# Kernel optimization log

Hardware: AMD Instinct MI355X
Metric: run time of the kernel (lower is better)

## Reference

```python
import jax, jax.numpy as jnp
import numpy as np

N = 50000        # nodes
E = 800000       # edges (before self loops)
IN = 128         # in_channels
HID = 32         # hidden_channels (per head)
HEADS = 4
OUT = 10         # out_channels (classes)
G = 64           # graphs in batch
NEG_SLOPE = 0.2  # PyG GATConv default leaky relu slope


def setup_inputs() -> dict:
    key = jax.random.key(0)
    ks = jax.random.split(key, 12)
    s = 0.05
    return {
        "x": jax.random.normal(ks[0], (N, IN), jnp.float32),
        "W1": jax.random.normal(ks[1], (IN, HEADS * HID), jnp.float32) * s,
        "a1_src": jax.random.normal(ks[2], (HEADS, HID), jnp.float32) * s,
        "a1_dst": jax.random.normal(ks[3], (HEADS, HID), jnp.float32) * s,
        "b1": jnp.zeros((HEADS * HID,), jnp.float32),
        "W2": jax.random.normal(ks[4], (HEADS * HID, HEADS * HID), jnp.float32) * s,
        "a2_src": jax.random.normal(ks[5], (HEADS, HID), jnp.float32) * s,
        "a2_dst": jax.random.normal(ks[6], (HEADS, HID), jnp.float32) * s,
        "b2": jnp.zeros((HEADS * HID,), jnp.float32),
        "Wl": jax.random.normal(ks[7], (HEADS * HID, OUT), jnp.float32) * s,
        "bl": jnp.zeros((OUT,), jnp.float32),
        "edge_index": jax.random.randint(ks[8], (2, E), 0, N, jnp.int32),
        "batch": jnp.sort(jax.random.randint(ks[9], (N,), 0, G, jnp.int32)),
    }


def gat_conv(x, src, dst, W, a_src, a_dst, b):
    """PyG GATConv (concat=True, self loops already in src/dst). Eval mode: no dropout."""
    n = x.shape[0]
    h = (x @ W).reshape(n, HEADS, HID)                       # [N,H,C]
    al_s = jnp.einsum('nhc,hc->nh', h, a_src)                # [N,H]
    al_d = jnp.einsum('nhc,hc->nh', h, a_dst)
    e = jax.nn.leaky_relu(al_s[src] + al_d[dst], NEG_SLOPE)  # [Etot,H]
    # segment softmax over destination node neighborhoods
    m = jax.ops.segment_max(e, dst, num_segments=n)
    m = jnp.where(jnp.isfinite(m), m, 0.0)
    p = jnp.exp(e - m[dst])
    z = jax.ops.segment_sum(p, dst, num_segments=n)
    alpha = p / (z[dst] + 1e-16)                             # [Etot,H]
    out = jax.ops.segment_sum(h[src] * alpha[:, :, None], dst, num_segments=n)
    return out.reshape(n, HEADS * HID) + b


def reference(x, W1, a1_src, a1_dst, b1, W2, a2_src, a2_dst, b2, Wl, bl,
              edge_index, batch):
    n = x.shape[0]
    loops = jnp.arange(n, dtype=edge_index.dtype)
    src = jnp.concatenate([edge_index[0], loops])
    dst = jnp.concatenate([edge_index[1], loops])

    h = jax.nn.elu(gat_conv(x, src, dst, W1, a1_src, a1_dst, b1))
    h = gat_conv(h, src, dst, W2, a2_src, a2_dst, b2)

    # global_mean_pool over graph ids
    counts = jax.ops.segment_sum(jnp.ones((n,), h.dtype), batch, num_segments=G)
    pooled = jax.ops.segment_sum(h, batch, num_segments=G) / jnp.maximum(counts, 1.0)[:, None]

    logits = pooled @ Wl + bl
    return jax.nn.softmax(logits, axis=1)
```

## Files before the change

kernel.cpp:

```cpp
#include <hip/hip_runtime.h>
#include <hip/hip_bf16.h>
#include <math.h>

#define HEADS 4
#define HID 32
#define FDIM 128
#define OUTC 10
#define NEG 0.2f
#define ECAP 512

typedef __attribute__((ext_vector_type(4))) float f32x4;
typedef __attribute__((ext_vector_type(8))) short bf16x8;

static __device__ __forceinline__ float lrelu(float v) { return v > 0.f ? v : NEG * v; }

static __device__ __forceinline__ unsigned bfr(float f) {
  unsigned u = __float_as_uint(f);
  return (u + 0x7fffu + ((u >> 16) & 1u)) >> 16;
}
static __device__ __forceinline__ float blo(unsigned u) { return __uint_as_float(u << 16); }
static __device__ __forceinline__ float bhi(unsigned u) { return __uint_as_float(u & 0xffff0000u); }

#define CHUNK 4096

__global__ __launch_bounds__(256) void k_bhist(
    const int* __restrict__ ei, int* __restrict__ gbc, int E, int n, int nb) {
  __shared__ int h[256];
  h[threadIdx.x] = 0;
  __syncthreads();
  int base = blockIdx.x * CHUNK;
  int tot = E + n;
  #pragma unroll
  for (int r = 0; r < 16; ++r) {
    int e = base + r * 256 + threadIdx.x;
    if (e < tot) {
      int dst = (e < E) ? ei[E + e] : (e - E);
      atomicAdd(&h[dst >> 8], 1);
    }
  }
  __syncthreads();
  if (threadIdx.x < nb && h[threadIdx.x]) atomicAdd(&gbc[threadIdx.x], h[threadIdx.x]);
}

__global__ void k_bscan(const int* __restrict__ gbc, int* __restrict__ bbase,
                        int* __restrict__ gbcur, int nb) {
  __shared__ int sh[256];
  int v = (threadIdx.x < nb) ? gbc[threadIdx.x] : 0;
  sh[threadIdx.x] = v;
  __syncthreads();
  #pragma unroll
  for (int off = 1; off < 256; off <<= 1) {
    int t = (threadIdx.x >= off) ? sh[threadIdx.x - off] : 0;
    __syncthreads();
    sh[threadIdx.x] += t;
    __syncthreads();
  }
  int excl = sh[threadIdx.x] - v;
  if (threadIdx.x <= nb) bbase[threadIdx.x] = excl;
  if (threadIdx.x < nb) gbcur[threadIdx.x] = excl;
}

__global__ __launch_bounds__(256) void k_bin(
    const int* __restrict__ ei, int* __restrict__ gbcur,
    int2* __restrict__ bbuf, int E, int n) {
  __shared__ int h[256];
  __shared__ int cur[256];
  h[threadIdx.x] = 0;
  __syncthreads();
  int base = blockIdx.x * CHUNK;
  int tot = E + n;
  #pragma unroll
  for (int r = 0; r < 16; ++r) {
    int e = base + r * 256 + threadIdx.x;
    if (e < tot) {
      int dst = (e < E) ? ei[E + e] : (e - E);
      atomicAdd(&h[dst >> 8], 1);
    }
  }
  __syncthreads();
  if (h[threadIdx.x]) cur[threadIdx.x] = atomicAdd(&gbcur[threadIdx.x], h[threadIdx.x]);
  __syncthreads();
  #pragma unroll
  for (int r = 0; r < 16; ++r) {
    int e = base + r * 256 + threadIdx.x;
    if (e < tot) {
      int src = (e < E) ? ei[e] : (e - E);
      int dst = (e < E) ? ei[E + e] : (e - E);
      int pos = atomicAdd(&cur[dst >> 8], 1);
      bbuf[pos] = make_int2(src, dst);
    }
  }
}

__global__ __launch_bounds__(256) void k_build(
    const int2* __restrict__ bbuf, const int* __restrict__ bbase,
    int* __restrict__ offs, int* __restrict__ csr, int* __restrict__ dpos,
    int n, int nb) {
  __shared__ int deg[256];
  __shared__ int sc[256];
  __shared__ int cur[256];
  int b = blockIdx.x;
  int ebeg = bbase[b], eend = bbase[b + 1];
  deg[threadIdx.x] = 0;
  __syncthreads();
  for (int i = ebeg + threadIdx.x; i < eend; i += 256)
    atomicAdd(&deg[bbuf[i].y & 255], 1);
  __syncthreads();
  int v = deg[threadIdx.x];
  sc[threadIdx.x] = v;
  __syncthreads();
  #pragma unroll
  for (int off = 1; off < 256; off <<= 1) {
    int t = (threadIdx.x >= off) ? sc[threadIdx.x - off] : 0;
    __syncthreads();
    sc[threadIdx.x] += t;
    __syncthreads();
  }
  int excl = sc[threadIdx.x] - v;
  int dst0 = b * 256 + threadIdx.x;
  if (dst0 < n) offs[dst0] = ebeg + excl;
  if (b == 0 && threadIdx.x == 0) offs[n] = bbase[nb];
  cur[threadIdx.x] = ebeg + excl;
  __syncthreads();
  for (int i = ebeg + threadIdx.x; i < eend; i += 256) {
    int2 sd = bbuf[i];
    int pos = atomicAdd(&cur[sd.y & 255], 1);
    csr[pos] = sd.x;
    dpos[pos] = sd.y;
  }
}

__global__ void k_wa(const float* __restrict__ W1, const float* __restrict__ W2,
                     const float* __restrict__ a1s, const float* __restrict__ a1d,
                     const float* __restrict__ a2s, const float* __restrict__ a2d,
                     float* __restrict__ Wa) {
  int layer = blockIdx.y;
  const float* W = layer ? W2 : W1;
  int c = blockIdx.x;
  int k = threadIdx.x;
  int h = c & 3;
  const float* av = (c < 4 ? (layer ? a2s : a1s) : (layer ? a2d : a1d)) + h * 32;
  const float* wr = W + (size_t)k * 128 + h * 32;
  float s = 0.f;
  #pragma unroll
  for (int j = 0; j < 32; j += 4) {
    float4 wv = *reinterpret_cast<const float4*>(wr + j);
    float4 a4 = *reinterpret_cast<const float4*>(av + j);
    s += wv.x * a4.x + wv.y * a4.y + wv.z * a4.z + wv.w * a4.w;
  }
  Wa[layer * 1024 + k * 8 + c] = s;
}

__global__ void k_prep(const float* __restrict__ W1, const float* __restrict__ W2,
                       const float* __restrict__ Wa, uint4* __restrict__ WF) {
  int layer = blockIdx.y;
  const float* W = layer ? W2 : W1;
  const float* wa = Wa + layer * 1024;
  int gid = blockIdx.x * 256 + threadIdx.x;
  if (gid >= 2304) return;
  int lane = gid & 63, frag = gid >> 6;
  int t = frag / 9, ct = frag - t * 9;
  int quad = lane >> 4, r = lane & 15;
  int kbase = t * 32 + quad * 8;
  unsigned v[8];
  if (ct < 8) {
    int col = ct * 16 + r;
    #pragma unroll
    for (int j = 0; j < 8; ++j) v[j] = bfr(W[(size_t)(kbase + j) * 128 + col]);
  } else if (r < 8) {
    #pragma unroll
    for (int j = 0; j < 8; ++j) v[j] = bfr(wa[(kbase + j) * 8 + r]);
  } else {
    #pragma unroll
    for (int j = 0; j < 8; ++j) v[j] = 0;
  }
  uint4 pk;
  pk.x = v[0] | (v[1] << 16);
  pk.y = v[2] | (v[3] << 16);
  pk.z = v[4] | (v[5] << 16);
  pk.w = v[6] | (v[7] << 16);
  WF[layer * 2304 + gid] = pk;
}

template<bool BF16IN>
__global__ __launch_bounds__(256) void k_mm(
    const void* __restrict__ Xv, const uint4* __restrict__ WF,
    unsigned short* __restrict__ H, float* __restrict__ AL, int n) {
  __shared__ uint4 wf[2304];
  int tid = threadIdx.x;
  #pragma unroll
  for (int i = 0; i < 9; ++i) wf[i * 256 + tid] = WF[i * 256 + tid];
  __syncthreads();
  int lane = tid & 63, wid = tid >> 6;
  int quad = lane >> 4, r = lane & 15;
  int rowbase = blockIdx.x * 64 + wid * 16;
  int arow = rowbase + r;
  int arowc = arow < n ? arow : 0;
  const bf16x8* wfs = (const bf16x8*)wf;

  f32x4 acc[9];
  #pragma unroll
  for (int ct = 0; ct < 9; ++ct) acc[ct] = 0;

  #pragma unroll
  for (int t = 0; t < 4; ++t) {
    bf16x8 a;
    if (BF16IN) {
      const uint4* xp = reinterpret_cast<const uint4*>(Xv) + (size_t)arowc * 16;
      uint4 u = xp[t * 4 + quad];
      a = *reinterpret_cast<const bf16x8*>(&u);
    } else {
      const float* xp = reinterpret_cast<const float*>(Xv) + (size_t)arowc * 128 + quad * 8;
      float4 x0 = *reinterpret_cast<const float4*>(xp + t * 32);
      float4 x1 = *reinterpret_cast<const float4*>(xp + t * 32 + 4);
      a[0] = (short)bfr(x0.x); a[1] = (short)bfr(x0.y);
      a[2] = (short)bfr(x0.z); a[3] = (short)bfr(x0.w);
      a[4] = (short)bfr(x1.x); a[5] = (short)bfr(x1.y);
      a[6] = (short)bfr(x1.z); a[7] = (short)bfr(x1.w);
    }
    #pragma unroll
    for (int ct = 0; ct < 9; ++ct)
      acc[ct] = __builtin_amdgcn_mfma_f32_16x16x32_bf16(
          a, wfs[(t * 9 + ct) * 64 + lane], acc[ct], 0, 0, 0);
  }

  int orow0 = rowbase + quad * 4;
  #pragma unroll
  for (int rr = 0; rr < 4; ++rr) {
    int orow = orow0 + rr;
    if (orow < n) {
      unsigned short* hp = H + (size_t)orow * 128 + r;
      #pragma unroll
      for (int ct = 0; ct < 8; ++ct) hp[ct * 16] = (unsigned short)bfr(acc[ct][rr]);
      if (r < 8) AL[(size_t)orow * 8 + r] = acc[8][rr];
    }
  }
}

template<bool ELU_OUT, bool POOL>
__global__ __launch_bounds__(256) void k_agg(
    const unsigned short* __restrict__ H, const float* __restrict__ AL,
    const int* __restrict__ offs, const int* __restrict__ csr,
    const int* __restrict__ dpos,
    const float* __restrict__ bias, unsigned short* __restrict__ OUT,
    const int* __restrict__ batch, float* __restrict__ pooled,
    int* __restrict__ gcnt, int n) {
  __shared__ __align__(16) char smem[ECAP * 4 + ECAP * 16];
  int* s_l = (int*)smem;
  float (*p_l)[4] = (float(*)[4])(smem + ECAP * 4);
  float (*o_l)[132] = (float(*)[132])smem;
  __shared__ int g_l[16];
  int tid = threadIdx.x;
  int lane = tid & 63;
  int r = lane & 15;
  int gg = (tid >> 6) * 4 + (lane >> 4);
  int nbase = blockIdx.x * 16;
  int node = nbase + gg;
  bool nvalid = node < n;
  int nodec = nvalid ? node : 0;
  int beg = offs[nodec];
  int end = nvalid ? offs[nodec + 1] : beg;
  int ebeg = offs[nbase];
  int eend = offs[min(nbase + 16, n)];
  int hsel = r >> 2;
  const uint4* hb = reinterpret_cast<const uint4*>(H) + r;

  if (POOL && r == 0) g_l[gg] = nvalid ? batch[node] : -1;

  float z = 0.f;
  float acc[8];
  #pragma unroll
  for (int k = 0; k < 8; ++k) acc[k] = 0.f;

  for (int c0 = ebeg; c0 < eend; c0 += ECAP) {
    int clen = min(ECAP, eend - c0);
    __syncthreads();
    for (int i = tid; i < clen; i += 256) {
      int s = csr[c0 + i];
      int d = dpos[c0 + i];
      float4 as_ = *reinterpret_cast<const float4*>(AL + (size_t)s * 8);
      float4 ad = *reinterpret_cast<const float4*>(AL + (size_t)d * 8 + 4);
      s_l[i] = s;
      float4 p;
      p.x = __expf(lrelu(as_.x + ad.x));
      p.y = __expf(lrelu(as_.y + ad.y));
      p.z = __expf(lrelu(as_.z + ad.z));
      p.w = __expf(lrelu(as_.w + ad.w));
      *reinterpret_cast<float4*>(&p_l[i][0]) = p;
    }
    __syncthreads();
    int lo = max(beg, c0), hi = min(end, c0 + clen);
    int cnt = hi - lo;
    int lbase = lo - c0;
    for (int j0 = 0; j0 < cnt; j0 += 4) {
      int j1 = j0 + 1, j2 = j0 + 2, j3 = j0 + 3;
      bool v1 = j1 < cnt, v2 = j2 < cnt, v3 = j3 < cnt;
      int jB = lbase + (v1 ? j1 : j0);
      int jC = lbase + (v2 ? j2 : j0);
      int jD = lbase + (v3 ? j3 : j0);
      int jA = lbase + j0;
      int sA = s_l[jA], sB = s_l[jB], sC = s_l[jC], sD = s_l[jD];
      float pA = p_l[jA][hsel];
      float pB = v1 ? p_l[jB][hsel] : 0.f;
      float pC = v2 ? p_l[jC][hsel] : 0.f;
      float pD = v3 ? p_l[jD][hsel] : 0.f;
      z += (pA + pB) + (pC + pD);
      uint4 uA = hb[(size_t)sA * 16];
      uint4 uB = hb[(size_t)sB * 16];
      uint4 uC = hb[(size_t)sC * 16];
      uint4 uD = hb[(size_t)sD * 16];
      acc[0] = fmaf(pA, blo(uA.x), acc[0]); acc[1] = fmaf(pA, bhi(uA.x), acc[1]);
      acc[2] = fmaf(pA, blo(uA.y), acc[2]); acc[3] = fmaf(pA, bhi(uA.y), acc[3]);
      acc[4] = fmaf(pA, blo(uA.z), acc[4]); acc[5] = fmaf(pA, bhi(uA.z), acc[5]);
      acc[6] = fmaf(pA, blo(uA.w), acc[6]); acc[7] = fmaf(pA, bhi(uA.w), acc[7]);
      acc[0] = fmaf(pB, blo(uB.x), acc[0]); acc[1] = fmaf(pB, bhi(uB.x), acc[1]);
      acc[2] = fmaf(pB, blo(uB.y), acc[2]); acc[3] = fmaf(pB, bhi(uB.y), acc[3]);
      acc[4] = fmaf(pB, blo(uB.z), acc[4]); acc[5] = fmaf(pB, bhi(uB.z), acc[5]);
      acc[6] = fmaf(pB, blo(uB.w), acc[6]); acc[7] = fmaf(pB, bhi(uB.w), acc[7]);
      acc[0] = fmaf(pC, blo(uC.x), acc[0]); acc[1] = fmaf(pC, bhi(uC.x), acc[1]);
      acc[2] = fmaf(pC, blo(uC.y), acc[2]); acc[3] = fmaf(pC, bhi(uC.y), acc[3]);
      acc[4] = fmaf(pC, blo(uC.z), acc[4]); acc[5] = fmaf(pC, bhi(uC.z), acc[5]);
      acc[6] = fmaf(pC, blo(uC.w), acc[6]); acc[7] = fmaf(pC, bhi(uC.w), acc[7]);
      acc[0] = fmaf(pD, blo(uD.x), acc[0]); acc[1] = fmaf(pD, bhi(uD.x), acc[1]);
      acc[2] = fmaf(pD, blo(uD.y), acc[2]); acc[3] = fmaf(pD, bhi(uD.y), acc[3]);
      acc[4] = fmaf(pD, blo(uD.z), acc[4]); acc[5] = fmaf(pD, bhi(uD.z), acc[5]);
      acc[6] = fmaf(pD, blo(uD.w), acc[6]); acc[7] = fmaf(pD, bhi(uD.w), acc[7]);
    }
  }

  float inv = 1.f / (z + 1e-16f);
  int f0 = r * 8;
  float4 b0 = *reinterpret_cast<const float4*>(bias + f0);
  float4 b1 = *reinterpret_cast<const float4*>(bias + f0 + 4);
  float o[8];
  o[0] = acc[0] * inv + b0.x; o[1] = acc[1] * inv + b0.y;
  o[2] = acc[2] * inv + b0.z; o[3] = acc[3] * inv + b0.w;
  o[4] = acc[4] * inv + b1.x; o[5] = acc[5] * inv + b1.y;
  o[6] = acc[6] * inv + b1.z; o[7] = acc[7] * inv + b1.w;
  if (ELU_OUT) {
    #pragma unroll
    for (int k = 0; k < 8; ++k) o[k] = o[k] > 0.f ? o[k] : expm1f(o[k]);
  }

  if (!POOL) {
    if (nvalid) {
      uint4 pk;
      pk.x = bfr(o[0]) | (bfr(o[1]) << 16);
      pk.y = bfr(o[2]) | (bfr(o[3]) << 16);
      pk.z = bfr(o[4]) | (bfr(o[5]) << 16);
      pk.w = bfr(o[6]) | (bfr(o[7]) << 16);
      reinterpret_cast<uint4*>(OUT)[(size_t)node * 16 + r] = pk;
    }
  } else {
    __syncthreads();
    *reinterpret_cast<float4*>(&o_l[gg][f0]) = make_float4(o[0], o[1], o[2], o[3]);
    *reinterpret_cast<float4*>(&o_l[gg][f0 + 4]) = make_float4(o[4], o[5], o[6], o[7]);
    __syncthreads();
    if (tid < 128) {
      int f = tid;
      float accp = 0.f; int cur = -1;
      #pragma unroll
      for (int i = 0; i < 16; ++i) {
        int g = g_l[i];
        if (g != cur) {
          if (cur >= 0) atomicAdd(&pooled[(size_t)cur * 128 + f], accp);
          cur = g; accp = 0.f;
        }
        if (g >= 0) accp += o_l[i][f];
      }
      if (cur >= 0) atomicAdd(&pooled[(size_t)cur * 128 + f], accp);
    } else if (tid == 128) {
      int cur = -1, c = 0;
      #pragma unroll
      for (int i = 0; i < 16; ++i) {
        int g = g_l[i];
        if (g != cur) { if (cur >= 0) atomicAdd(&gcnt[cur], c); cur = g; c = 0; }
        if (g >= 0) ++c;
      }
      if (cur >= 0) atomicAdd(&gcnt[cur], c);
    }
  }
}

__global__ void k_head(const float* __restrict__ pooled, const int* __restrict__ gcnt,
                       const float* __restrict__ Wl, const float* __restrict__ bl,
                       float* __restrict__ out) {
  int g = blockIdx.x;
  int lane = threadIdx.x;
  float cnt = fmaxf((float)gcnt[g], 1.f);
  float pA = pooled[(size_t)g * 128 + lane] / cnt;
  float pB = pooled[(size_t)g * 128 + lane + 64] / cnt;
  float l[OUTC];
  #pragma unroll
  for (int o = 0; o < OUTC; ++o) {
    float s = pA * Wl[lane * OUTC + o] + pB * Wl[(lane + 64) * OUTC + o];
    #pragma unroll
    for (int off = 32; off; off >>= 1) s += __shfl_xor(s, off);
    l[o] = s + bl[o];
  }
  float mx = l[0];
  #pragma unroll
  for (int o = 1; o < OUTC; ++o) mx = fmaxf(mx, l[o]);
  float se = 0.f;
  #pragma unroll
  for (int o = 0; o < OUTC; ++o) { l[o] = __expf(l[o] - mx); se += l[o]; }
  if (lane == 0) {
    float inv = 1.f / se;
    #pragma unroll
    for (int o = 0; o < OUTC; ++o) out[g * OUTC + o] = l[o] * inv;
  }
}

extern "C" void kernel_launch(void* const* d_in, const int* in_sizes, int n_in,
                              void* d_out, int out_size, void* d_ws, size_t ws_size,
                              hipStream_t stream) {
  const float* x   = (const float*)d_in[0];
  const float* W1  = (const float*)d_in[1];
  const float* a1s = (const float*)d_in[2];
  const float* a1d = (const float*)d_in[3];
  const float* b1  = (const float*)d_in[4];
  const float* W2  = (const float*)d_in[5];
  const float* a2s = (const float*)d_in[6];
  const float* a2d = (const float*)d_in[7];
  const float* b2  = (const float*)d_in[8];
  const float* Wl  = (const float*)d_in[9];
  const float* bl  = (const float*)d_in[10];
  const int* ei    = (const int*)d_in[11];
  const int* batch = (const int*)d_in[12];
  const int N = in_sizes[12];
  const int E = in_sizes[11] / 2;
  const int G = out_size / OUTC;
  float* out = (float*)d_out;
  (void)n_in; (void)ws_size;

  const int tot = E + N;
  const int NB = (N + 255) / 256;

  char* w = (char*)d_ws;
  auto alloc = [&](size_t bytes) { char* p = w; w += (bytes + 255) & ~(size_t)255; return (void*)p; };
  unsigned short* H = (unsigned short*)alloc((size_t)N * FDIM * sizeof(unsigned short));
  unsigned short* ACT = (unsigned short*)alloc((size_t)N * FDIM * sizeof(unsigned short));
  float* AL     = (float*)alloc((size_t)N * 8 * sizeof(float));
  uint4* WF     = (uint4*)alloc(2 * 2304 * sizeof(uint4));
  float* Wa     = (float*)alloc(2 * 1024 * sizeof(float));
  int*   offs   = (int*)alloc((size_t)(N + 1) * sizeof(int));
  int*   csr    = (int*)alloc((size_t)tot * sizeof(int));
  int*   dpos   = (int*)alloc((size_t)tot * sizeof(int));
  int2*  bbuf   = (int2*)alloc((size_t)tot * sizeof(int2));
  int*   bbase  = (int*)alloc((size_t)(NB + 1) * sizeof(int));
  int*   gbcur  = (int*)alloc(256 * sizeof(int));
  char* z0 = w;
  int*   gbc    = (int*)alloc(256 * sizeof(int));
  int*   gcnt   = (int*)alloc((size_t)G * sizeof(int));
  float* pooled = (float*)alloc((size_t)G * FDIM * sizeof(float));
  size_t zbytes = (size_t)(w - z0);
  hipMemsetAsync(z0, 0, zbytes, stream);

  int ab4 = (tot + CHUNK - 1) / CHUNK;
  k_bhist<<<ab4, 256, 0, stream>>>(ei, gbc, E, N, NB);
  k_bscan<<<1, 256, 0, stream>>>(gbc, bbase, gbcur, NB);
  k_bin<<<ab4, 256, 0, stream>>>(ei, gbcur, bbuf, E, N);
  k_build<<<NB, 256, 0, stream>>>(bbuf, bbase, offs, csr, dpos, N, NB);

  k_wa<<<dim3(8, 2), 128, 0, stream>>>(W1, W2, a1s, a1d, a2s, a2d, Wa);
  k_prep<<<dim3(9, 2), 256, 0, stream>>>(W1, W2, Wa, WF);

  int gb = (N + 63) / 64;
  int ab = (N + 15) / 16;
  k_mm<false><<<gb, 256, 0, stream>>>(x, WF, H, AL, N);
  k_agg<true, false><<<ab, 256, 0, stream>>>(H, AL, offs, csr, dpos, b1, ACT, batch, pooled, gcnt, N);
  k_mm<true><<<gb, 256, 0, stream>>>(ACT, WF + 2304, H, AL, N);
  k_agg<false, true><<<ab, 256, 0, stream>>>(H, AL, offs, csr, dpos, b2, nullptr, batch, pooled, gcnt, N);

  k_head<<<G, 64, 0, stream>>>(pooled, gcnt, Wl, bl, out);
}
```

Measured before the change: 240.1 us.

## Fold scan and weight-prep kernels into consumers, reshape matmul and gather loops

Removes the separate bucket-scan kernel by having each binning and build block redo the 256-entry scan locally, with gbcur now zeroed and holding relative offsets. Merges the attention-weight projection into the prep kernel through shared memory, which drops two launches. The matmul now reads weight fragments straight from global/L2 instead of staging them in LDS, and the unrolled loop is replaced by a per-step fragment preload. The aggregation loop is widened to 8 gathers in flight per iteration. The trade-offs are redundant scan work in every block, possible L2 pressure from weight reads, and higher register use.

```diff
diff --git a/kernel.cpp b/kernel.cpp
--- a/kernel.cpp
+++ b/kernel.cpp
@@ -42,47 +42,42 @@
   if (threadIdx.x < nb && h[threadIdx.x]) atomicAdd(&gbc[threadIdx.x], h[threadIdx.x]);
 }
 
-__global__ void k_bscan(const int* __restrict__ gbc, int* __restrict__ bbase,
-                        int* __restrict__ gbcur, int nb) {
-  __shared__ int sh[256];
-  int v = (threadIdx.x < nb) ? gbc[threadIdx.x] : 0;
-  sh[threadIdx.x] = v;
-  __syncthreads();
-  #pragma unroll
-  for (int off = 1; off < 256; off <<= 1) {
-    int t = (threadIdx.x >= off) ? sh[threadIdx.x - off] : 0;
-    __syncthreads();
-    sh[threadIdx.x] += t;
-    __syncthreads();
-  }
-  int excl = sh[threadIdx.x] - v;
-  if (threadIdx.x <= nb) bbase[threadIdx.x] = excl;
-  if (threadIdx.x < nb) gbcur[threadIdx.x] = excl;
-}
-
 __global__ __launch_bounds__(256) void k_bin(
-    const int* __restrict__ ei, int* __restrict__ gbcur,
-    int2* __restrict__ bbuf, int E, int n) {
+    const int* __restrict__ ei, const int* __restrict__ gbc,
+    int* __restrict__ gbcur, int2* __restrict__ bbuf, int E, int n) {
   __shared__ int h[256];
+  __shared__ int sc[256];
   __shared__ int cur[256];
-  h[threadIdx.x] = 0;
+  int tid = threadIdx.x;
+  h[tid] = 0;
   __syncthreads();
   int base = blockIdx.x * CHUNK;
   int tot = E + n;
   #pragma unroll
   for (int r = 0; r < 16; ++r) {
-    int e = base + r * 256 + threadIdx.x;
+    int e = base + r * 256 + tid;
     if (e < tot) {
       int dst = (e < E) ? ei[E + e] : (e - E);
       atomicAdd(&h[dst >> 8], 1);
     }
   }
   __syncthreads();
-  if (h[threadIdx.x]) cur[threadIdx.x] = atomicAdd(&gbcur[threadIdx.x], h[threadIdx.x]);
+  int v = gbc[tid];
+  sc[tid] = v;
+  __syncthreads();
+  #pragma unroll
+  for (int off = 1; off < 256; off <<= 1) {
+    int t = (tid >= off) ? sc[tid - off] : 0;
+    __syncthreads();
+    sc[tid] += t;
+    __syncthreads();
+  }
+  int lbase = sc[tid] - v;
+  if (h[tid]) cur[tid] = lbase + atomicAdd(&gbcur[tid], h[tid]);
   __syncthreads();
   #pragma unroll
   for (int r = 0; r < 16; ++r) {
-    int e = base + r * 256 + threadIdx.x;
+    int e = base + r * 256 + tid;
     if (e < tot) {
       int src = (e < E) ? ei[e] : (e - E);
       int dst = (e < E) ? ei[E + e] : (e - E);
@@ -93,36 +88,50 @@
 }
 
 __global__ __launch_bounds__(256) void k_build(
-    const int2* __restrict__ bbuf, const int* __restrict__ bbase,
+    const int2* __restrict__ bbuf, const int* __restrict__ gbc,
     int* __restrict__ offs, int* __restrict__ csr, int* __restrict__ dpos,
     int n, int nb) {
+  __shared__ int scb[256];
   __shared__ int deg[256];
   __shared__ int sc[256];
   __shared__ int cur[256];
+  __shared__ int sbase[2];
   int b = blockIdx.x;
-  int ebeg = bbase[b], eend = bbase[b + 1];
-  deg[threadIdx.x] = 0;
-  __syncthreads();
-  for (int i = ebeg + threadIdx.x; i < eend; i += 256)
+  int tid = threadIdx.x;
+  int vb = gbc[tid];
+  scb[tid] = vb;
+  __syncthreads();
+  #pragma unroll
+  for (int off = 1; off < 256; off <<= 1) {
+    int t = (tid >= off) ? scb[tid - off] : 0;
+    __syncthreads();
+    scb[tid] += t;
+    __syncthreads();
+  }
+  if (tid == b) { sbase[0] = scb[tid] - vb; sbase[1] = scb[tid]; }
+  if (b == 0 && tid == nb - 1) offs[n] = scb[tid];
+  deg[tid] = 0;
+  __syncthreads();
+  int ebeg = sbase[0], eend = sbase[1];
+  for (int i = ebeg + tid; i < eend; i += 256)
     atomicAdd(&deg[bbuf[i].y & 255], 1);
   __syncthreads();
-  int v = deg[threadIdx.x];
-  sc[threadIdx.x] = v;
+  int v = deg[tid];
+  sc[tid] = v;
   __syncthreads();
   #pragma unroll
   for (int off = 1; off < 256; off <<= 1) {
-    int t = (threadIdx.x >= off) ? sc[threadIdx.x - off] : 0;
-    __syncthreads();
-    sc[threadIdx.x] += t;
-    __syncthreads();
-  }
-  int excl = sc[threadIdx.x] - v;
-  int dst0 = b * 256 + threadIdx.x;
+    int t = (tid >= off) ? sc[tid - off] : 0;
+    __syncthreads();
+    sc[tid] += t;
+    __syncthreads();
+  }
+  int excl = sc[tid] - v;
+  int dst0 = b * 256 + tid;
   if (dst0 < n) offs[dst0] = ebeg + excl;
-  if (b == 0 && threadIdx.x == 0) offs[n] = bbase[nb];
-  cur[threadIdx.x] = ebeg + excl;
-  __syncthreads();
-  for (int i = ebeg + threadIdx.x; i < eend; i += 256) {
+  cur[tid] = ebeg + excl;
+  __syncthreads();
+  for (int i = ebeg + tid; i < eend; i += 256) {
     int2 sd = bbuf[i];
     int pos = atomicAdd(&cur[sd.y & 255], 1);
     csr[pos] = sd.x;
@@ -130,33 +139,33 @@
   }
 }
 
-__global__ void k_wa(const float* __restrict__ W1, const float* __restrict__ W2,
-                     const float* __restrict__ a1s, const float* __restrict__ a1d,
-                     const float* __restrict__ a2s, const float* __restrict__ a2d,
-                     float* __restrict__ Wa) {
+__global__ __launch_bounds__(256) void k_prep(
+    const float* __restrict__ W1, const float* __restrict__ W2,
+    const float* __restrict__ a1s, const float* __restrict__ a1d,
+    const float* __restrict__ a2s, const float* __restrict__ a2d,
+    uint4* __restrict__ WF) {
   int layer = blockIdx.y;
   const float* W = layer ? W2 : W1;
-  int c = blockIdx.x;
-  int k = threadIdx.x;
-  int h = c & 3;
-  const float* av = (c < 4 ? (layer ? a2s : a1s) : (layer ? a2d : a1d)) + h * 32;
-  const float* wr = W + (size_t)k * 128 + h * 32;
-  float s = 0.f;
-  #pragma unroll
-  for (int j = 0; j < 32; j += 4) {
-    float4 wv = *reinterpret_cast<const float4*>(wr + j);
-    float4 a4 = *reinterpret_cast<const float4*>(av + j);
-    s += wv.x * a4.x + wv.y * a4.y + wv.z * a4.z + wv.w * a4.w;
-  }
-  Wa[layer * 1024 + k * 8 + c] = s;
-}
-
-__global__ void k_prep(const float* __restrict__ W1, const float* __restrict__ W2,
-                       const float* __restrict__ Wa, uint4* __restrict__ WF) {
-  int layer = blockIdx.y;
-  const float* W = layer ? W2 : W1;
-  const float* wa = Wa + layer * 1024;
-  int gid = blockIdx.x * 256 + threadIdx.x;
+  __shared__ float wa[128][8];
+  int tid = threadIdx.x;
+  #pragma unroll
+  for (int q = 0; q < 4; ++q) {
+    int e = tid * 4 + q;
+    int k = e >> 3, c = e & 7;
+    int h = c & 3;
+    const float* av = (c < 4 ? (layer ? a2s : a1s) : (layer ? a2d : a1d)) + h * 32;
+    const float* wr = W + (size_t)k * 128 + h * 32;
+    float s = 0.f;
+    #pragma unroll
+    for (int j = 0; j < 32; j += 4) {
+      float4 wv = *reinterpret_cast<const float4*>(wr + j);
+      float4 a4 = *reinterpret_cast<const float4*>(av + j);
+      s += wv.x * a4.x + wv.y * a4.y + wv.z * a4.z + wv.w * a4.w;
+    }
+    wa[k][c] = s;
+  }
+  __syncthreads();
+  int gid = blockIdx.x * 256 + tid;
   if (gid >= 2304) return;
   int lane = gid & 63, frag = gid >> 6;
   int t = frag / 9, ct = frag - t * 9;
@@ -169,7 +178,7 @@
     for (int j = 0; j < 8; ++j) v[j] = bfr(W[(size_t)(kbase + j) * 128 + col]);
   } else if (r < 8) {
     #pragma unroll
-    for (int j = 0; j < 8; ++j) v[j] = bfr(wa[(kbase + j) * 8 + r]);
+    for (int j = 0; j < 8; ++j) v[j] = bfr(wa[kbase + j][r]);
   } else {
     #pragma unroll
     for (int j = 0; j < 8; ++j) v[j] = 0;
@@ -186,23 +195,19 @@
 __global__ __launch_bounds__(256) void k_mm(
     const void* __restrict__ Xv, const uint4* __restrict__ WF,
     unsigned short* __restrict__ H, float* __restrict__ AL, int n) {
-  __shared__ uint4 wf[2304];
   int tid = threadIdx.x;
-  #pragma unroll
-  for (int i = 0; i < 9; ++i) wf[i * 256 + tid] = WF[i * 256 + tid];
-  __syncthreads();
   int lane = tid & 63, wid = tid >> 6;
   int quad = lane >> 4, r = lane & 15;
   int rowbase = blockIdx.x * 64 + wid * 16;
   int arow = rowbase + r;
   int arowc = arow < n ? arow : 0;
-  const bf16x8* wfs = (const bf16x8*)wf;
+  const bf16x8* wfs = (const bf16x8*)WF;
 
   f32x4 acc[9];
   #pragma unroll
   for (int ct = 0; ct < 9; ++ct) acc[ct] = 0;
 
-  #pragma unroll
+  #pragma unroll 1
   for (int t = 0; t < 4; ++t) {
     bf16x8 a;
     if (BF16IN) {
@@ -218,10 +223,12 @@
       a[4] = (short)bfr(x1.x); a[5] = (short)bfr(x1.y);
       a[6] = (short)bfr(x1.z); a[7] = (short)bfr(x1.w);
     }
+    bf16x8 bfr_[9];
+    #pragma unroll
+    for (int ct = 0; ct < 9; ++ct) bfr_[ct] = wfs[(t * 9 + ct) * 64 + lane];
     #pragma unroll
     for (int ct = 0; ct < 9; ++ct)
-      acc[ct] = __builtin_amdgcn_mfma_f32_16x16x32_bf16(
-          a, wfs[(t * 9 + ct) * 64 + lane], acc[ct], 0, 0, 0);
+      acc[ct] = __builtin_amdgcn_mfma_f32_16x16x32_bf16(a, bfr_[ct], acc[ct], 0, 0, 0);
   }
 
   int orow0 = rowbase + quad * 4;
@@ -292,39 +299,30 @@
     int lo = max(beg, c0), hi = min(end, c0 + clen);
     int cnt = hi - lo;
     int lbase = lo - c0;
-    for (int j0 = 0; j0 < cnt; j0 += 4) {
-      int j1 = j0 + 1, j2 = j0 + 2, j3 = j0 + 3;
-      bool v1 = j1 < cnt, v2 = j2 < cnt, v3 = j3 < cnt;
-      int jB = lbase + (v1 ? j1 : j0);
-      int jC = lbase + (v2 ? j2 : j0);
-      int jD = lbase + (v3 ? j3 : j0);
-      int jA = lbase + j0;
-      int sA = s_l[jA], sB = s_l[jB], sC = s_l[jC], sD = s_l[jD];
-      float pA = p_l[jA][hsel];
-      float pB = v1 ? p_l[jB][hsel] : 0.f;
-      float pC = v2 ? p_l[jC][hsel] : 0.f;
-      float pD = v3 ? p_l[jD][hsel] : 0.f;
-      z += (pA + pB) + (pC + pD);
-      uint4 uA = hb[(size_t)sA * 16];
-      uint4 uB = hb[(size_t)sB * 16];
-      uint4 uC = hb[(size_t)sC * 16];
-      uint4 uD = hb[(size_t)sD * 16];
-      acc[0] = fmaf(pA, blo(uA.x), acc[0]); acc[1] = fmaf(pA, bhi(uA.x), acc[1]);
-      acc[2] = fmaf(pA, blo(uA.y), acc[2]); acc[3] = fmaf(pA, bhi(uA.y), acc[3]);
-      acc[4] = fmaf(pA, blo(uA.z), acc[4]); acc[5] = fmaf(pA, bhi(uA.z), acc[5]);
-      acc[6] = fmaf(pA, blo(uA.w), acc[6]); acc[7] = fmaf(pA, bhi(uA.w), acc[7]);
-      acc[0] = fmaf(pB, blo(uB.x), acc[0]); acc[1] = fmaf(pB, bhi(uB.x), acc[1]);
-      acc[2] = fmaf(pB, blo(uB.y), acc[2]); acc[3] = fmaf(pB, bhi(uB.y), acc[3]);
-      acc[4] = fmaf(pB, blo(uB.z), acc[4]); acc[5] = fmaf(pB, bhi(uB.z), acc[5]);
-      acc[6] = fmaf(pB, blo(uB.w), acc[6]); acc[7] = fmaf(pB, bhi(uB.w), acc[7]);
-      acc[0] = fmaf(pC, blo(uC.x), acc[0]); acc[1] = fmaf(pC, bhi(uC.x), acc[1]);
-      acc[2] = fmaf(pC, blo(uC.y), acc[2]); acc[3] = fmaf(pC, bhi(uC.y), acc[3]);
-      acc[4] = fmaf(pC, blo(uC.z), acc[4]); acc[5] = fmaf(pC, bhi(uC.z), acc[5]);
-      acc[6] = fmaf(pC, blo(uC.w), acc[6]); acc[7] = fmaf(pC, bhi(uC.w), acc[7]);
-      acc[0] = fmaf(pD, blo(uD.x), acc[0]); acc[1] = fmaf(pD, bhi(uD.x), acc[1]);
-      acc[2] = fmaf(pD, blo(uD.y), acc[2]); acc[3] = fmaf(pD, bhi(uD.y), acc[3]);
-      acc[4] = fmaf(pD, blo(uD.z), acc[4]); acc[5] = fmaf(pD, bhi(uD.z), acc[5]);
-      acc[6] = fmaf(pD, blo(uD.w), acc[6]); acc[7] = fmaf(pD, bhi(uD.w), acc[7]);
+    for (int j0 = 0; j0 < cnt; j0 += 8) {
+      int ss[8]; float pp[8];
+      #pragma unroll
+      for (int u = 0; u < 8; ++u) {
+        int j = j0 + u;
+        bool vu = j < cnt;
+        int jc = lbase + (vu ? j : j0);
+        ss[u] = s_l[jc];
+        float pv = p_l[jc][hsel];
+        pp[u] = vu ? pv : 0.f;
+      }
+      uint4 uu[8];
+      #pragma unroll
+      for (int u = 0; u < 8; ++u) uu[u] = hb[(size_t)ss[u] * 16];
+      #pragma unroll
+      for (int u = 0; u < 8; ++u) {
+        float p = pp[u];
+        z += p;
+        uint4 q = uu[u];
+        acc[0] = fmaf(p, blo(q.x), acc[0]); acc[1] = fmaf(p, bhi(q.x), acc[1]);
+        acc[2] = fmaf(p, blo(q.y), acc[2]); acc[3] = fmaf(p, bhi(q.y), acc[3]);
+        acc[4] = fmaf(p, blo(q.z), acc[4]); acc[5] = fmaf(p, bhi(q.z), acc[5]);
+        acc[6] = fmaf(p, blo(q.w), acc[6]); acc[7] = fmaf(p, bhi(q.w), acc[7]);
+      }
     }
   }
 
@@ -442,15 +440,13 @@
   unsigned short* ACT = (unsigned short*)alloc((size_t)N * FDIM * sizeof(unsigned short));
   float* AL     = (float*)alloc((size_t)N * 8 * sizeof(float));
   uint4* WF     = (uint4*)alloc(2 * 2304 * sizeof(uint4));
-  float* Wa     = (float*)alloc(2 * 1024 * sizeof(float));
   int*   offs   = (int*)alloc((size_t)(N + 1) * sizeof(int));
   int*   csr    = (int*)alloc((size_t)tot * sizeof(int));
   int*   dpos   = (int*)alloc((size_t)tot * sizeof(int));
   int2*  bbuf   = (int2*)alloc((size_t)tot * sizeof(int2));
-  int*   bbase  = (int*)alloc((size_t)(NB + 1) * sizeof(int));
-  int*   gbcur  = (int*)alloc(256 * sizeof(int));
   char* z0 = w;
   int*   gbc    = (int*)alloc(256 * sizeof(int));
+  int*   gbcur  = (int*)alloc(256 * sizeof(int));
   int*   gcnt   = (int*)alloc((size_t)G * sizeof(int));
   float* pooled = (float*)alloc((size_t)G * FDIM * sizeof(float));
   size_t zbytes = (size_t)(w - z0);
@@ -458,12 +454,10 @@
 
   int ab4 = (tot + CHUNK - 1) / CHUNK;
   k_bhist<<<ab4, 256, 0, stream>>>(ei, gbc, E, N, NB);
-  k_bscan<<<1, 256, 0, stream>>>(gbc, bbase, gbcur, NB);
-  k_bin<<<ab4, 256, 0, stream>>>(ei, gbcur, bbuf, E, N);
-  k_build<<<NB, 256, 0, stream>>>(bbuf, bbase, offs, csr, dpos, N, NB);
-
-  k_wa<<<dim3(8, 2), 128, 0, stream>>>(W1, W2, a1s, a1d, a2s, a2d, Wa);
-  k_prep<<<dim3(9, 2), 256, 0, stream>>>(W1, W2, Wa, WF);
+  k_bin<<<ab4, 256, 0, stream>>>(ei, gbc, gbcur, bbuf, E, N);
+  k_build<<<NB, 256, 0, stream>>>(bbuf, gbc, offs, csr, dpos, N, NB);
+
+  k_prep<<<dim3(9, 2), 256, 0, stream>>>(W1, W2, a1s, a1d, a2s, a2d, WF);
 
   int gb = (N + 63) / 64;
   int ab = (N + 15) / 16;
```

Result: slower. 250.2 us (+4.2%).
